# Kernel tuning notes

Hardware: AMD Instinct MI355X
Metric: run time of the kernel (lower is better)

## Reference

```python
import jax, jax.numpy as jnp
import numpy as np

NUM_USERS = 80000
NUM_ITEMS = 40000
N_NODES = NUM_USERS + NUM_ITEMS
EMB = 128
NNZ = 600000
BATCH = 4096
N_LAYERS = 3


def setup_inputs() -> dict:
    key = jax.random.key(0)
    ks = jax.random.split(key, 8)
    users = jax.random.randint(ks[0], (BATCH,), 0, NUM_USERS)
    pos_items = jax.random.randint(ks[1], (BATCH,), 0, NUM_ITEMS)
    neg_items = jax.random.randint(ks[2], (BATCH,), 0, NUM_ITEMS)
    user_emb = jax.random.normal(ks[3], (NUM_USERS, EMB), dtype=jnp.float32)
    item_emb = jax.random.normal(ks[4], (NUM_ITEMS, EMB), dtype=jnp.float32)
    adj_row = jax.random.randint(ks[5], (NNZ,), 0, N_NODES)
    adj_col = jax.random.randint(ks[6], (NNZ,), 0, N_NODES)
    adj_val = jax.random.uniform(ks[7], (NNZ,), dtype=jnp.float32)
    return {
        "users": users, "pos_items": pos_items, "neg_items": neg_items,
        "user_emb": user_emb, "item_emb": item_emb,
        "adj_row": adj_row, "adj_col": adj_col, "adj_val": adj_val,
        "n_layers": N_LAYERS,
    }


def _spmm(row, col, val, x, n_nodes):
    # sparse (COO) adjacency @ dense x : [N, D]
    return jax.ops.segment_sum(val[:, None] * x[col], row, num_segments=n_nodes)


def reference(users, pos_items, neg_items, user_emb, item_emb, adj_row, adj_col, adj_val, n_layers):
    num_users = user_emb.shape[0]
    n_nodes = num_users + item_emb.shape[0]
    ego = jnp.concatenate([user_emb, item_emb], axis=0)  # [N, D]
    acc = ego
    h = ego
    for _ in range(n_layers):
        h = _spmm(adj_row, adj_col, adj_val, h, n_nodes)
        acc = acc + h
    final = acc / jnp.asarray(n_layers + 1, dtype=acc.dtype)  # mean over layer stack
    u_g = final[:num_users]
    i_g = final[num_users:]
    return (u_g[users], i_g[pos_items], i_g[neg_items], i_g)
```

## Files before the change

### kernel.cpp

```cpp
#include <hip/hip_runtime.h>
#include <hip/hip_fp16.h>

#define EMB      128
#define NUSERS   80000
#define NITEMS   40000
#define NNODES   120000
#define NNZV     600000
#define BATCHN   4096
#define WELL     24
#define CSTR     16

typedef unsigned int u32;

__device__ __forceinline__ u32 pack2(float lo, float hi) {
    u32 a = __float_as_uint(lo), b = __float_as_uint(hi);
    a = (a + 0x7FFFu + ((a >> 16) & 1u)) >> 16;
    b = (b + 0x7FFFu + ((b >> 16) & 1u)) >> 16;
    return a | (b << 16);
}
__device__ __forceinline__ float lo2f(u32 u) { return __uint_as_float(u << 16); }
__device__ __forceinline__ float hi2f(u32 u) { return __uint_as_float(u & 0xFFFF0000u); }

__device__ __forceinline__ float val15(u32 w) {
    return __half2float(__ushort_as_half((unsigned short)(w & 0x7FFFu)));
}

#define CVT_N   (NNODES * EMB / 8)
#define FILL_N  (NNODES * CSTR / 4)
#define EBLKS   ((NNZV + 255) / 256)
#define CVBLKS  ((CVT_N + 255) / 256)

__global__ __launch_bounds__(256) void zero_counts(uint4* __restrict__ counts4)
{
    int stride = gridDim.x * 256;
    for (int i = blockIdx.x * 256 + threadIdx.x; i < FILL_N; i += stride)
        counts4[i] = make_uint4(0, 0, 0, 0);
}

__global__ __launch_bounds__(256) void convert_build(
    const int* __restrict__ row, const int* __restrict__ col,
    const float* __restrict__ val,
    int* __restrict__ counts, u32* __restrict__ ell,
    const float* __restrict__ ue, const float* __restrict__ ie,
    u32* __restrict__ ego)
{
    if (blockIdx.x < EBLKS) {
        int e = blockIdx.x * 256 + threadIdx.x;
        if (e >= NNZV) return;
        int r = row[e];
        int s = atomicAdd(&counts[(size_t)r << 4], 1);
        if (s < WELL) {
            u32 entry = ((u32)col[e] << 15)
                      | (u32)__half_as_ushort(__float2half_rn(val[e]));
            ell[(size_t)r * WELL + s] = entry;
        }
    } else {
        int t = (blockIdx.x - EBLKS) * 256 + threadIdx.x;
        if (t >= CVT_N) return;
        const float4* s = (t < NUSERS * EMB / 8)
            ? ((const float4*)ue) + (size_t)t * 2
            : ((const float4*)ie) + ((size_t)t - NUSERS * EMB / 8) * 2;
        float4 a = s[0], b = s[1];
        uint4 o;
        o.x = pack2(a.x, a.y); o.y = pack2(a.z, a.w);
        o.z = pack2(b.x, b.y); o.w = pack2(b.z, b.w);
        ((uint4*)ego)[t] = o;
    }
}

__device__ __forceinline__ void gath8(
    const u32* __restrict__ src, const u32* __restrict__ e, u32 voff,
    int k0, int c, float& a0, float& a1)
{
    u32 w0 = e[0], w1 = e[1], w2 = e[2], w3 = e[3];
    u32 w4 = e[4], w5 = e[5], w6 = e[6], w7 = e[7];
    const u32* p0 = src + ((size_t)min(w0 >> 15, NNODES - 1u) << 6);
    const u32* p1 = src + ((size_t)min(w1 >> 15, NNODES - 1u) << 6);
    const u32* p2 = src + ((size_t)min(w2 >> 15, NNODES - 1u) << 6);
    const u32* p3 = src + ((size_t)min(w3 >> 15, NNODES - 1u) << 6);
    const u32* p4 = src + ((size_t)min(w4 >> 15, NNODES - 1u) << 6);
    const u32* p5 = src + ((size_t)min(w5 >> 15, NNODES - 1u) << 6);
    const u32* p6 = src + ((size_t)min(w6 >> 15, NNODES - 1u) << 6);
    const u32* p7 = src + ((size_t)min(w7 >> 15, NNODES - 1u) << 6);
    u32 x0, x1, x2, x3, x4, x5, x6, x7;
    asm volatile(
        "global_load_dword %[x0], %[v], %[s0]\n\t"
        "global_load_dword %[x1], %[v], %[s1]\n\t"
        "global_load_dword %[x2], %[v], %[s2]\n\t"
        "global_load_dword %[x3], %[v], %[s3]\n\t"
        "global_load_dword %[x4], %[v], %[s4]\n\t"
        "global_load_dword %[x5], %[v], %[s5]\n\t"
        "global_load_dword %[x6], %[v], %[s6]\n\t"
        "global_load_dword %[x7], %[v], %[s7]\n\t"
        "s_waitcnt vmcnt(0)"
        : [x0]"=&v"(x0), [x1]"=&v"(x1), [x2]"=&v"(x2), [x3]"=&v"(x3),
          [x4]"=&v"(x4), [x5]"=&v"(x5), [x6]"=&v"(x6), [x7]"=&v"(x7)
        : [v]"v"(voff),
          [s0]"s"(p0), [s1]"s"(p1), [s2]"s"(p2), [s3]"s"(p3),
          [s4]"s"(p4), [s5]"s"(p5), [s6]"s"(p6), [s7]"s"(p7)
        : "memory");
    float v0 = (k0 + 0 < c) ? val15(w0) : 0.f;
    float v1 = (k0 + 1 < c) ? val15(w1) : 0.f;
    float v2 = (k0 + 2 < c) ? val15(w2) : 0.f;
    float v3 = (k0 + 3 < c) ? val15(w3) : 0.f;
    float v4 = (k0 + 4 < c) ? val15(w4) : 0.f;
    float v5 = (k0 + 5 < c) ? val15(w5) : 0.f;
    float v6 = (k0 + 6 < c) ? val15(w6) : 0.f;
    float v7 = (k0 + 7 < c) ? val15(w7) : 0.f;
    a0 += v0*lo2f(x0) + v1*lo2f(x1) + v2*lo2f(x2) + v3*lo2f(x3)
        + v4*lo2f(x4) + v5*lo2f(x5) + v6*lo2f(x6) + v7*lo2f(x7);
    a1 += v0*hi2f(x0) + v1*hi2f(x1) + v2*hi2f(x2) + v3*hi2f(x3)
        + v4*hi2f(x4) + v5*hi2f(x5) + v6*hi2f(x6) + v7*hi2f(x7);
}

__device__ __forceinline__ float2 row_accum(
    int r, u32 voff, const int* __restrict__ counts,
    const u32* __restrict__ ell, const u32* __restrict__ src)
{
    const u32* e = ell + (size_t)r * WELL;
    int c = min(counts[(size_t)r << 4], WELL);
    float a0 = 0.f, a1 = 0.f;
    gath8(src, e, voff, 0, c, a0, a1);
    if (c > 8) {
        gath8(src, e + 8, voff, 8, c, a0, a1);
        if (c > 16)
            gath8(src, e + 16, voff, 16, c, a0, a1);
    }
    return make_float2(a0, a1);
}

__global__ __launch_bounds__(256) void spmm_ell(
    const int* __restrict__ counts, const u32* __restrict__ ell,
    const u32* __restrict__ src, u32* __restrict__ dst)
{
    int wid = (blockIdx.x * 256 + threadIdx.x) >> 6;
    int r = __builtin_amdgcn_readfirstlane(wid);
    int lane = threadIdx.x & 63;
    float2 a = row_accum(r, lane * 4, counts, ell, src);
    dst[((size_t)r << 6) + lane] = pack2(a.x, a.y);
}

__global__ __launch_bounds__(256) void spmm3_finalize(
    const int* __restrict__ users,
    const int* __restrict__ counts, const u32* __restrict__ ell,
    const float* __restrict__ ue, const float* __restrict__ ie,
    const u32* __restrict__ h1, const u32* __restrict__ h2,
    float* __restrict__ out)
{
    int wid = (blockIdx.x * 256 + threadIdx.x) >> 6;
    int w = __builtin_amdgcn_readfirstlane(wid);
    int lane = threadIdx.x & 63;
    int r = (w < BATCHN) ? users[w] : NUSERS + (w - BATCHN);
    float2 a = row_accum(r, lane * 4, counts, ell, h2);
    const float2* eg = (r < NUSERS)
        ? (const float2*)(ue + (size_t)r * EMB)
        : (const float2*)(ie + (size_t)(r - NUSERS) * EMB);
    float2 g = eg[lane];
    u32 b1 = h1[((size_t)r << 6) + lane];
    u32 b2 = h2[((size_t)r << 6) + lane];
    float2 o;
    o.x = (g.x + lo2f(b1) + lo2f(b2) + a.x) * 0.25f;
    o.y = (g.y + hi2f(b1) + hi2f(b2) + a.y) * 0.25f;
    float2* dst = (w < BATCHN)
        ? (float2*)out + (size_t)w * 64
        : (float2*)(out + (size_t)3 * BATCHN * EMB) + (size_t)(w - BATCHN) * 64;
    dst[lane] = o;
}

__global__ __launch_bounds__(256) void gather_pn(
    const int* __restrict__ pos, const int* __restrict__ neg,
    const float* __restrict__ ig, float* __restrict__ out)
{
    int b = blockIdx.x * 8 + (threadIdx.x >> 5);
    int lane = threadIdx.x & 31;
    int idx = (b < BATCHN) ? pos[b] : neg[b - BATCHN];
    float4 x = ((const float4*)(ig + (size_t)idx * EMB))[lane];
    ((float4*)(out + (size_t)(BATCHN + b) * EMB))[lane] = x;
}

extern "C" void kernel_launch(void* const* d_in, const int* in_sizes, int n_in,
                              void* d_out, int out_size, void* d_ws, size_t ws_size,
                              hipStream_t stream)
{
    const int*   users = (const int*)d_in[0];
    const int*   pos   = (const int*)d_in[1];
    const int*   neg   = (const int*)d_in[2];
    const float* ue    = (const float*)d_in[3];
    const float* ie    = (const float*)d_in[4];
    const int*   arow  = (const int*)d_in[5];
    const int*   acol  = (const int*)d_in[6];
    const float* aval  = (const float*)d_in[7];

    const size_t hU = (size_t)NNODES * 64;
    char* ws = (char*)d_ws;
    u32* h2     = (u32*)ws;  ws += hU * sizeof(u32);
    u32* h1     = (u32*)ws;  ws += hU * sizeof(u32);
    u32* ego    = (u32*)ws;  ws += hU * sizeof(u32);
    u32* ell    = (u32*)ws;  ws += (size_t)NNODES * WELL * sizeof(u32);
    int* counts = (int*)ws;  ws += (size_t)NNODES * CSTR * sizeof(int);

    zero_counts<<<1024, 256, 0, stream>>>((uint4*)counts);

    convert_build<<<EBLKS + CVBLKS, 256, 0, stream>>>(
        arow, acol, aval, counts, ell, ue, ie, ego);

    spmm_ell<<<NNODES / 4, 256, 0, stream>>>(counts, ell, ego, h1);
    spmm_ell<<<NNODES / 4, 256, 0, stream>>>(counts, ell, h1, h2);

    float* out = (float*)d_out;
    spmm3_finalize<<<(BATCHN + NITEMS) / 4, 256, 0, stream>>>(
        users, counts, ell, ue, ie, h1, h2, out);

    float* ig = out + (size_t)3 * BATCHN * EMB;
    gather_pn<<<(2 * BATCHN) / 8, 256, 0, stream>>>(pos, neg, ig, out);
}
```

Before: 132.2 us.

## Build ELL via two-pass row-bucket sort, fold pos/neg gathers into finalize

Replaces the global-atomic per-row ELL build, which needed a padded zeroed counts array, with a two-pass bucketing scheme. Edges are first binned into 512-row buckets using shared-memory histograms and one global atomic per bucket. A second kernel then scatters each bucket into ELL using shared-memory counters. The finalize kernel now also recomputes the pos/neg item rows directly instead of running a separate gather, which removes a launch and a dependent pass at the cost of redundant SpMM work. Bucket capacity is fixed (BCAP), so overflow would silently drop edges, and the ELL slot order is nondeterministic.

```diff
diff --git a/kernel.cpp b/kernel.cpp
--- a/kernel.cpp
+++ b/kernel.cpp
@@ -8,7 +8,13 @@
 #define NNZV     600000
 #define BATCHN   4096
 #define WELL     24
-#define CSTR     16
+
+#define NBKT     256
+#define BSHIFT   9
+#define BCAP     3328
+#define EPB      8192
+#define NBBLK    ((NNZV + EPB - 1) / EPB)
+#define NBUCK    ((NNODES + 511) >> 9)
 
 typedef unsigned int u32;
 
@@ -20,42 +26,55 @@
 }
 __device__ __forceinline__ float lo2f(u32 u) { return __uint_as_float(u << 16); }
 __device__ __forceinline__ float hi2f(u32 u) { return __uint_as_float(u & 0xFFFF0000u); }
-
 __device__ __forceinline__ float val15(u32 w) {
     return __half2float(__ushort_as_half((unsigned short)(w & 0x7FFFu)));
 }
 
 #define CVT_N   (NNODES * EMB / 8)
-#define FILL_N  (NNODES * CSTR / 4)
-#define EBLKS   ((NNZV + 255) / 256)
-#define CVBLKS  ((CVT_N + 255) / 256)
-
-__global__ __launch_bounds__(256) void zero_counts(uint4* __restrict__ counts4)
-{
-    int stride = gridDim.x * 256;
-    for (int i = blockIdx.x * 256 + threadIdx.x; i < FILL_N; i += stride)
-        counts4[i] = make_uint4(0, 0, 0, 0);
-}
-
-__global__ __launch_bounds__(256) void convert_build(
+#define CVBLKS  ((CVT_N + 1023) / 1024)
+
+__global__ __launch_bounds__(1024) void bucket_convert(
     const int* __restrict__ row, const int* __restrict__ col,
     const float* __restrict__ val,
-    int* __restrict__ counts, u32* __restrict__ ell,
+    int* __restrict__ gcount, uint2* __restrict__ bkt,
     const float* __restrict__ ue, const float* __restrict__ ie,
     u32* __restrict__ ego)
 {
-    if (blockIdx.x < EBLKS) {
-        int e = blockIdx.x * 256 + threadIdx.x;
-        if (e >= NNZV) return;
-        int r = row[e];
-        int s = atomicAdd(&counts[(size_t)r << 4], 1);
-        if (s < WELL) {
-            u32 entry = ((u32)col[e] << 15)
-                      | (u32)__half_as_ushort(__float2half_rn(val[e]));
-            ell[(size_t)r * WELL + s] = entry;
+    if (blockIdx.x < NBBLK) {
+        __shared__ u32 hist[NBKT];
+        __shared__ u32 base[NBKT];
+        int tid = threadIdx.x;
+        if (tid < NBKT) hist[tid] = 0;
+        __syncthreads();
+        u32 packA[8], cc[8], rk[8];
+        int bb[8];
+        #pragma unroll
+        for (int k = 0; k < 8; ++k) {
+            int e = blockIdx.x * EPB + k * 1024 + tid;
+            bool ok = e < NNZV;
+            int r  = ok ? row[e] : 0;
+            int c  = ok ? col[e] : 0;
+            float v = ok ? val[e] : 0.f;
+            packA[k] = ((u32)r << 15)
+                     | (u32)(__half_as_ushort(__float2half_rn(v)) & 0x7FFF);
+            cc[k] = (u32)c;
+            bb[k] = ok ? (r >> BSHIFT) : -1;
+            rk[k] = ok ? atomicAdd(&hist[r >> BSHIFT], 1u) : 0u;
+        }
+        __syncthreads();
+        if (tid < NBKT)
+            base[tid] = hist[tid] ? (u32)atomicAdd(&gcount[tid], (int)hist[tid]) : 0u;
+        __syncthreads();
+        #pragma unroll
+        for (int k = 0; k < 8; ++k) {
+            if (bb[k] >= 0) {
+                u32 pos = base[bb[k]] + rk[k];
+                if (pos < BCAP)
+                    bkt[(size_t)bb[k] * BCAP + pos] = make_uint2(packA[k], cc[k]);
+            }
         }
     } else {
-        int t = (blockIdx.x - EBLKS) * 256 + threadIdx.x;
+        int t = (blockIdx.x - NBBLK) * 1024 + threadIdx.x;
         if (t >= CVT_N) return;
         const float4* s = (t < NUSERS * EMB / 8)
             ? ((const float4*)ue) + (size_t)t * 2
@@ -66,6 +85,28 @@
         o.z = pack2(b.x, b.y); o.w = pack2(b.z, b.w);
         ((uint4*)ego)[t] = o;
     }
+}
+
+__global__ __launch_bounds__(1024) void ell_from_buckets(
+    const int* __restrict__ gcount, const uint2* __restrict__ bkt,
+    u32* __restrict__ ell, int* __restrict__ counts)
+{
+    __shared__ int cnt[512];
+    int b = blockIdx.x;
+    int tid = threadIdx.x;
+    if (tid < 512) cnt[tid] = 0;
+    __syncthreads();
+    int nb = min(gcount[b], BCAP);
+    for (int i = tid; i < nb; i += 1024) {
+        uint2 e = bkt[(size_t)b * BCAP + i];
+        u32 r = e.x >> 15;
+        int s = atomicAdd(&cnt[r & 511], 1);
+        if (s < WELL)
+            ell[(size_t)r * WELL + s] = (e.y << 15) | (e.x & 0x7FFFu);
+    }
+    __syncthreads();
+    int gr = (b << BSHIFT) + tid;
+    if (tid < 512 && gr < NNODES) counts[gr] = cnt[tid];
 }
 
 __device__ __forceinline__ void gath8(
@@ -118,7 +159,7 @@
     const u32* __restrict__ ell, const u32* __restrict__ src)
 {
     const u32* e = ell + (size_t)r * WELL;
-    int c = min(counts[(size_t)r << 4], WELL);
+    int c = min(counts[r], WELL);
     float a0 = 0.f, a1 = 0.f;
     gath8(src, e, voff, 0, c, a0, a1);
     if (c > 8) {
@@ -140,8 +181,10 @@
     dst[((size_t)r << 6) + lane] = pack2(a.x, a.y);
 }
 
+#define TOTW (2 * BATCHN + NITEMS + BATCHN)
 __global__ __launch_bounds__(256) void spmm3_finalize(
-    const int* __restrict__ users,
+    const int* __restrict__ users, const int* __restrict__ pos,
+    const int* __restrict__ neg,
     const int* __restrict__ counts, const u32* __restrict__ ell,
     const float* __restrict__ ue, const float* __restrict__ ie,
     const u32* __restrict__ h1, const u32* __restrict__ h2,
@@ -150,7 +193,14 @@
     int wid = (blockIdx.x * 256 + threadIdx.x) >> 6;
     int w = __builtin_amdgcn_readfirstlane(wid);
     int lane = threadIdx.x & 63;
-    int r = (w < BATCHN) ? users[w] : NUSERS + (w - BATCHN);
+    int r, d;
+    if (w < BATCHN)                        { r = users[w];                      d = w; }
+    else if (w < BATCHN + NITEMS)          { int i = w - BATCHN;
+                                             r = NUSERS + i;                   d = 3 * BATCHN + i; }
+    else if (w < 2 * BATCHN + NITEMS)      { int i = w - BATCHN - NITEMS;
+                                             r = NUSERS + pos[i];              d = BATCHN + i; }
+    else                                   { int i = w - 2 * BATCHN - NITEMS;
+                                             r = NUSERS + neg[i];              d = 2 * BATCHN + i; }
     float2 a = row_accum(r, lane * 4, counts, ell, h2);
     const float2* eg = (r < NUSERS)
         ? (const float2*)(ue + (size_t)r * EMB)
@@ -161,21 +211,7 @@
     float2 o;
     o.x = (g.x + lo2f(b1) + lo2f(b2) + a.x) * 0.25f;
     o.y = (g.y + hi2f(b1) + hi2f(b2) + a.y) * 0.25f;
-    float2* dst = (w < BATCHN)
-        ? (float2*)out + (size_t)w * 64
-        : (float2*)(out + (size_t)3 * BATCHN * EMB) + (size_t)(w - BATCHN) * 64;
-    dst[lane] = o;
-}
-
-__global__ __launch_bounds__(256) void gather_pn(
-    const int* __restrict__ pos, const int* __restrict__ neg,
-    const float* __restrict__ ig, float* __restrict__ out)
-{
-    int b = blockIdx.x * 8 + (threadIdx.x >> 5);
-    int lane = threadIdx.x & 31;
-    int idx = (b < BATCHN) ? pos[b] : neg[b - BATCHN];
-    float4 x = ((const float4*)(ig + (size_t)idx * EMB))[lane];
-    ((float4*)(out + (size_t)(BATCHN + b) * EMB))[lane] = x;
+    ((float2*)out + (size_t)d * 64)[lane] = o;
 }
 
 extern "C" void kernel_launch(void* const* d_in, const int* in_sizes, int n_in,
@@ -193,24 +229,24 @@
 
     const size_t hU = (size_t)NNODES * 64;
     char* ws = (char*)d_ws;
-    u32* h2     = (u32*)ws;  ws += hU * sizeof(u32);
-    u32* h1     = (u32*)ws;  ws += hU * sizeof(u32);
-    u32* ego    = (u32*)ws;  ws += hU * sizeof(u32);
-    u32* ell    = (u32*)ws;  ws += (size_t)NNODES * WELL * sizeof(u32);
-    int* counts = (int*)ws;  ws += (size_t)NNODES * CSTR * sizeof(int);
-
-    zero_counts<<<1024, 256, 0, stream>>>((uint4*)counts);
-
-    convert_build<<<EBLKS + CVBLKS, 256, 0, stream>>>(
-        arow, acol, aval, counts, ell, ue, ie, ego);
+    u32*   h2     = (u32*)ws;   ws += hU * sizeof(u32);
+    u32*   h1     = (u32*)ws;   ws += hU * sizeof(u32);
+    u32*   ego    = (u32*)ws;   ws += hU * sizeof(u32);
+    u32*   ell    = (u32*)ws;   ws += (size_t)NNODES * WELL * sizeof(u32);
+    uint2* bkt    = (uint2*)ws; ws += (size_t)NBKT * BCAP * sizeof(uint2);
+    int*   counts = (int*)ws;   ws += NNODES * sizeof(int);
+    int*   gcount = (int*)ws;   ws += NBKT * sizeof(int);
+
+    hipMemsetAsync(gcount, 0, NBKT * sizeof(int), stream);
+
+    bucket_convert<<<NBBLK + CVBLKS, 1024, 0, stream>>>(
+        arow, acol, aval, gcount, bkt, ue, ie, ego);
+
+    ell_from_buckets<<<NBUCK, 1024, 0, stream>>>(gcount, bkt, ell, counts);
 
     spmm_ell<<<NNODES / 4, 256, 0, stream>>>(counts, ell, ego, h1);
     spmm_ell<<<NNODES / 4, 256, 0, stream>>>(counts, ell, h1, h2);
 
-    float* out = (float*)d_out;
-    spmm3_finalize<<<(BATCHN + NITEMS) / 4, 256, 0, stream>>>(
-        users, counts, ell, ue, ie, h1, h2, out);
-
-    float* ig = out + (size_t)3 * BATCHN * EMB;
-    gather_pn<<<(2 * BATCHN) / 8, 256, 0, stream>>>(pos, neg, ig, out);
-}
+    spmm3_finalize<<<TOTW / 4, 256, 0, stream>>>(
+        users, pos, neg, counts, ell, ue, ie, h1, h2, (float*)d_out);
+}
```

After: 113.8 us. -14.0%, faster.
